# Kernel optimization log

Measured on AMD Instinct MI355X. Metric: run time of the kernel, lower is better.

Reference implementation:

```python
import jax, jax.numpy as jnp
import numpy as np

NUM_CLASSES = 10
N = 4194304  # 2**22 samples


def setup_inputs() -> dict:
    key = jax.random.key(0)
    k1, k2 = jax.random.split(key)
    outputs = jax.random.uniform(k1, (N, NUM_CLASSES), dtype=jnp.float32)
    target = jax.random.randint(k2, (N,), 0, NUM_CLASSES, dtype=jnp.int64)
    return {"outputs": outputs, "target": target}


def reference(outputs, target):
    # y = one-hot(target) with 10 classes, float
    y = jax.nn.one_hot(target, NUM_CLASSES, dtype=outputs.dtype)  # [N, 10]
    # sum_j (outputs @ y.T)[i, j] == outputs[i] . sum_j y[j]
    # identical math to torch.sum(torch.mm(outputs, y.t()), dim=1) without the [N, N] intermediate
    col_counts = jnp.sum(y, axis=0)                 # [10] class counts
    nominator = outputs @ col_counts                # [N]
    denominator = jnp.linalg.norm(outputs) * jnp.linalg.norm(y)  # Frobenius norms
    return jnp.mean(-jnp.log(nominator / denominator))
```

## Files before the change

kernel.cpp:

```cpp
#include <hip/hip_runtime.h>
#include <math.h>

#define NUM_CLASSES 10
#define A_BLOCKS 512
#define B_BLOCKS 2048


__global__ void __launch_bounds__(256) hist_kernel(const int* __restrict__ target,
                                                   unsigned int* __restrict__ pc, int n) {
    unsigned int cnt[NUM_CLASSES];
#pragma unroll
    for (int c = 0; c < NUM_CLASSES; ++c) cnt[c] = 0u;

    const int tid = blockIdx.x * blockDim.x + threadIdx.x;
    const int stride = gridDim.x * blockDim.x;
    const int4* __restrict__ t4 = (const int4*)target;
    const int n4 = n >> 2;

    for (int i = tid; i < n4; i += stride) {
        int4 v = t4[i];
#pragma unroll
        for (int c = 0; c < NUM_CLASSES; ++c) {
            cnt[c] += (unsigned int)(v.x == c) + (unsigned int)(v.y == c) +
                      (unsigned int)(v.z == c) + (unsigned int)(v.w == c);
        }
    }

#pragma unroll
    for (int c = 0; c < NUM_CLASSES; ++c) {
        unsigned int v = cnt[c];
        for (int off = 32; off > 0; off >>= 1)
            v += (unsigned int)__shfl_down((int)v, off, 64);
        cnt[c] = v;
    }

    __shared__ unsigned int sh[4][NUM_CLASSES];
    const int wave = threadIdx.x >> 6;
    if ((threadIdx.x & 63) == 0) {
#pragma unroll
        for (int c = 0; c < NUM_CLASSES; ++c) sh[wave][c] = cnt[c];
    }
    __syncthreads();
    if (threadIdx.x < NUM_CLASSES) {
        const int c = threadIdx.x;
        pc[blockIdx.x * NUM_CLASSES + c] = sh[0][c] + sh[1][c] + sh[2][c] + sh[3][c];
    }
}

__global__ void __launch_bounds__(256) main_kernel(const float* __restrict__ outputs,
                                                   const unsigned int* __restrict__ pc,
                                                   float2* __restrict__ pacc, int n) {
    const int wave = threadIdx.x >> 6;
    const int lane = threadIdx.x & 63;

    unsigned int pw[NUM_CLASSES];
#pragma unroll
    for (int c = 0; c < NUM_CLASSES; ++c) pw[c] = 0u;
#pragma unroll
    for (int r = 0; r < A_BLOCKS / 256; ++r) {
        const unsigned int* row = pc + (threadIdx.x + r * 256) * NUM_CLASSES;
#pragma unroll
        for (int c = 0; c < NUM_CLASSES; ++c) pw[c] += row[c];
    }
#pragma unroll
    for (int c = 0; c < NUM_CLASSES; ++c) {
        unsigned int v = pw[c];
        for (int off = 32; off > 0; off >>= 1)
            v += (unsigned int)__shfl_down((int)v, off, 64);
        pw[c] = v;
    }
    __shared__ unsigned int shw[4][NUM_CLASSES];
    __shared__ float fw[NUM_CLASSES];
    if (lane == 0) {
#pragma unroll
        for (int c = 0; c < NUM_CLASSES; ++c) shw[wave][c] = pw[c];
    }
    __syncthreads();
    if (threadIdx.x < NUM_CLASSES) {
        const int c = threadIdx.x;
        fw[c] = (float)(shw[0][c] + shw[1][c] + shw[2][c] + shw[3][c]);
    }
    __syncthreads();
    float w[NUM_CLASSES];
#pragma unroll
    for (int c = 0; c < NUM_CLASSES; ++c) w[c] = fw[c];

    __shared__ float4 stage4[4][320];
    const float4* __restrict__ o4 = (const float4*)outputs;
    const int nchunks = n >> 7;
    const int nwaves = gridDim.x * 4;
    const int gwave = blockIdx.x * 4 + wave;
    const int iters = (nchunks + nwaves - 1) / nwaves;

    float sum_log = 0.f, sumsq = 0.f;
    for (int it = 0; it < iters; ++it) {
        const int ch = gwave + it * nwaves;
        const bool valid = ch < nchunks;
        float4 v0, v1, v2, v3, v4;
        if (valid) {
            const size_t b4 = (size_t)ch * 320;
            v0 = o4[b4 + 0 * 64 + lane];
            v1 = o4[b4 + 1 * 64 + lane];
            v2 = o4[b4 + 2 * 64 + lane];
            v3 = o4[b4 + 3 * 64 + lane];
            v4 = o4[b4 + 4 * 64 + lane];
        }
        __syncthreads();
        if (valid) {
            stage4[wave][0 * 64 + lane] = v0;
            stage4[wave][1 * 64 + lane] = v1;
            stage4[wave][2 * 64 + lane] = v2;
            stage4[wave][3 * 64 + lane] = v3;
            stage4[wave][4 * 64 + lane] = v4;
        }
        __syncthreads();
        if (valid) {
            const float4* sp = (const float4*)((const float*)&stage4[wave][0] + lane * 20);
            float4 a = sp[0], b = sp[1], c4 = sp[2], d = sp[3], e = sp[4];
            float r0[NUM_CLASSES] = {a.x, a.y, a.z, a.w, b.x, b.y, b.z, b.w, c4.x, c4.y};
            float r1[NUM_CLASSES] = {c4.z, c4.w, d.x, d.y, d.z, d.w, e.x, e.y, e.z, e.w};
            float nom0 = 0.f, nom1 = 0.f;
#pragma unroll
            for (int c = 0; c < NUM_CLASSES; ++c) {
                nom0 += r0[c] * w[c];
                nom1 += r1[c] * w[c];
                sumsq += r0[c] * r0[c] + r1[c] * r1[c];
            }
            sum_log += __logf(nom0) + __logf(nom1);
        }
    }

    for (int off = 32; off > 0; off >>= 1) {
        sum_log += __shfl_down(sum_log, off, 64);
        sumsq += __shfl_down(sumsq, off, 64);
    }
    __shared__ float s1[4], s2[4];
    if (lane == 0) { s1[wave] = sum_log; s2[wave] = sumsq; }
    __syncthreads();
    if (threadIdx.x == 0) {
        float t1 = s1[0] + s1[1] + s1[2] + s1[3];
        float t2 = s2[0] + s2[1] + s2[2] + s2[3];
        pacc[blockIdx.x] = make_float2(t1, t2);
    }
}

__global__ void __launch_bounds__(256) finalize_kernel(const float2* __restrict__ pacc,
                                                       float* __restrict__ out, float fn) {
    float sum_log = 0.f, sumsq = 0.f;
    for (int i = threadIdx.x; i < B_BLOCKS; i += 256) {
        float2 v = pacc[i];
        sum_log += v.x;
        sumsq += v.y;
    }
    for (int off = 32; off > 0; off >>= 1) {
        sum_log += __shfl_down(sum_log, off, 64);
        sumsq += __shfl_down(sumsq, off, 64);
    }
    __shared__ float s1[4], s2[4];
    const int wave = threadIdx.x >> 6;
    if ((threadIdx.x & 63) == 0) { s1[wave] = sum_log; s2[wave] = sumsq; }
    __syncthreads();
    if (threadIdx.x == 0) {
        float t1 = s1[0] + s1[1] + s1[2] + s1[3];
        float t2 = s2[0] + s2[1] + s2[2] + s2[3];
        out[0] = 0.5f * logf(t2) + 0.5f * logf(fn) - t1 / fn;
    }
}

extern "C" void kernel_launch(void* const* d_in, const int* in_sizes, int n_in,
                              void* d_out, int out_size, void* d_ws, size_t ws_size,
                              hipStream_t stream) {
    const float* outputs = (const float*)d_in[0];
    const int* target = (const int*)d_in[1];
    const int n = in_sizes[1];

    unsigned int* pc = (unsigned int*)d_ws;
    float2* pacc = (float2*)((char*)d_ws + A_BLOCKS * NUM_CLASSES * sizeof(unsigned int));

    hist_kernel<<<A_BLOCKS, 256, 0, stream>>>(target, pc, n);
    main_kernel<<<B_BLOCKS, 256, 0, stream>>>(outputs, pc, pacc, n);
    finalize_kernel<<<1, 256, 0, stream>>>(pacc, (float*)d_out, (float)n);
}
```

Before: 250.6 us.

## Load outputs directly into LDS and fuse finalize via last-block reduction

Replaces the register-staged global loads and LDS stores with global_load_lds builtins that write 16-byte chunks straight into shared memory. It removes the separate finalize kernel by having the last block, found with an atomic counter, do the final reduction. It also changes the grid to 1792 blocks with a launch-bounds occupancy hint of 7. The aim is to cut register traffic, one kernel launch, and tail overhead, at the cost of relying on the direct-to-LDS load layout and adding atomic/fence overhead.

```diff
diff --git a/kernel.cpp b/kernel.cpp
--- a/kernel.cpp
+++ b/kernel.cpp
@@ -3,11 +3,14 @@
 
 #define NUM_CLASSES 10
 #define A_BLOCKS 512
-#define B_BLOCKS 2048
+#define B_BLOCKS 1792
 
 
 __global__ void __launch_bounds__(256) hist_kernel(const int* __restrict__ target,
-                                                   unsigned int* __restrict__ pc, int n) {
+                                                   unsigned int* __restrict__ pc,
+                                                   unsigned int* __restrict__ done, int n) {
+    if (blockIdx.x == 0 && threadIdx.x == 0) *done = 0u;
+
     unsigned int cnt[NUM_CLASSES];
 #pragma unroll
     for (int c = 0; c < NUM_CLASSES; ++c) cnt[c] = 0u;
@@ -47,9 +50,12 @@
     }
 }
 
-__global__ void __launch_bounds__(256) main_kernel(const float* __restrict__ outputs,
-                                                   const unsigned int* __restrict__ pc,
-                                                   float2* __restrict__ pacc, int n) {
+__global__ void __launch_bounds__(256, 7) main_kernel(const float* __restrict__ outputs,
+                                                      const unsigned int* __restrict__ pc,
+                                                      float2* __restrict__ pacc,
+                                                      unsigned int* __restrict__ done,
+                                                      float* __restrict__ out,
+                                                      int n, float fn) {
     const int wave = threadIdx.x >> 6;
     const int lane = threadIdx.x & 63;
 
@@ -96,22 +102,17 @@
     for (int it = 0; it < iters; ++it) {
         const int ch = gwave + it * nwaves;
         const bool valid = ch < nchunks;
-        float4 v0, v1, v2, v3, v4;
+        __syncthreads();
         if (valid) {
             const size_t b4 = (size_t)ch * 320;
-            v0 = o4[b4 + 0 * 64 + lane];
-            v1 = o4[b4 + 1 * 64 + lane];
-            v2 = o4[b4 + 2 * 64 + lane];
-            v3 = o4[b4 + 3 * 64 + lane];
-            v4 = o4[b4 + 4 * 64 + lane];
-        }
-        __syncthreads();
-        if (valid) {
-            stage4[wave][0 * 64 + lane] = v0;
-            stage4[wave][1 * 64 + lane] = v1;
-            stage4[wave][2 * 64 + lane] = v2;
-            stage4[wave][3 * 64 + lane] = v3;
-            stage4[wave][4 * 64 + lane] = v4;
+#pragma unroll
+            for (int k = 0; k < 5; ++k) {
+                __builtin_amdgcn_global_load_lds(
+                    (const __attribute__((address_space(1))) unsigned int*)(o4 + b4 + k * 64 + lane),
+                    (__attribute__((address_space(3))) unsigned int*)(unsigned long)(unsigned long long)
+                        (unsigned long long)(uintptr_t)&stage4[wave][k * 64],
+                    16, 0, 0);
+            }
         }
         __syncthreads();
         if (valid) {
@@ -137,33 +138,36 @@
     __shared__ float s1[4], s2[4];
     if (lane == 0) { s1[wave] = sum_log; s2[wave] = sumsq; }
     __syncthreads();
+    __shared__ bool amLast;
     if (threadIdx.x == 0) {
-        float t1 = s1[0] + s1[1] + s1[2] + s1[3];
-        float t2 = s2[0] + s2[1] + s2[2] + s2[3];
-        pacc[blockIdx.x] = make_float2(t1, t2);
+        pacc[blockIdx.x] = make_float2(s1[0] + s1[1] + s1[2] + s1[3],
+                                       s2[0] + s2[1] + s2[2] + s2[3]);
+        __threadfence();
+        unsigned int t = atomicAdd(done, 1u);
+        amLast = (t == gridDim.x - 1);
     }
-}
+    __syncthreads();
 
-__global__ void __launch_bounds__(256) finalize_kernel(const float2* __restrict__ pacc,
-                                                       float* __restrict__ out, float fn) {
-    float sum_log = 0.f, sumsq = 0.f;
-    for (int i = threadIdx.x; i < B_BLOCKS; i += 256) {
-        float2 v = pacc[i];
-        sum_log += v.x;
-        sumsq += v.y;
-    }
-    for (int off = 32; off > 0; off >>= 1) {
-        sum_log += __shfl_down(sum_log, off, 64);
-        sumsq += __shfl_down(sumsq, off, 64);
-    }
-    __shared__ float s1[4], s2[4];
-    const int wave = threadIdx.x >> 6;
-    if ((threadIdx.x & 63) == 0) { s1[wave] = sum_log; s2[wave] = sumsq; }
-    __syncthreads();
-    if (threadIdx.x == 0) {
-        float t1 = s1[0] + s1[1] + s1[2] + s1[3];
-        float t2 = s2[0] + s2[1] + s2[2] + s2[3];
-        out[0] = 0.5f * logf(t2) + 0.5f * logf(fn) - t1 / fn;
+    if (amLast) {
+        __threadfence();
+        float t1 = 0.f, t2 = 0.f;
+        for (int i = threadIdx.x; i < B_BLOCKS; i += 256) {
+            float2 v = pacc[i];
+            t1 += v.x;
+            t2 += v.y;
+        }
+        for (int off = 32; off > 0; off >>= 1) {
+            t1 += __shfl_down(t1, off, 64);
+            t2 += __shfl_down(t2, off, 64);
+        }
+        __syncthreads();
+        if (lane == 0) { s1[wave] = t1; s2[wave] = t2; }
+        __syncthreads();
+        if (threadIdx.x == 0) {
+            float a1 = s1[0] + s1[1] + s1[2] + s1[3];
+            float a2 = s2[0] + s2[1] + s2[2] + s2[3];
+            out[0] = 0.5f * logf(a2) + 0.5f * logf(fn) - a1 / fn;
+        }
     }
 }
 
@@ -175,9 +179,9 @@
     const int n = in_sizes[1];
 
     unsigned int* pc = (unsigned int*)d_ws;
-    float2* pacc = (float2*)((char*)d_ws + A_BLOCKS * NUM_CLASSES * sizeof(unsigned int));
+    float2* pacc = (float2*)((char*)d_ws + 20480);
+    unsigned int* done = (unsigned int*)((char*)d_ws + 34816);
 
-    hist_kernel<<<A_BLOCKS, 256, 0, stream>>>(target, pc, n);
-    main_kernel<<<B_BLOCKS, 256, 0, stream>>>(outputs, pc, pacc, n);
-    finalize_kernel<<<1, 256, 0, stream>>>(pacc, (float*)d_out, (float)n);
+    hist_kernel<<<A_BLOCKS, 256, 0, stream>>>(target, pc, done, n);
+    main_kernel<<<B_BLOCKS, 256, 0, stream>>>(outputs, pc, pacc, done, (float*)d_out, n, (float)n);
 }
```

Result: slower. 328.9 us (+31.2%).
